# Optimization experiments

Hardware: AMD Instinct MI355X
Metric: run time of the kernel (lower is better)

Reference implementation:

```python
import math
import jax, jax.numpy as jnp
import numpy as np

S, D = 4096, 2048
H, DH = 16, 128
ROPE_BASE = 10000.0


def _rotate_half(x):
    # x: [..., dh]; pairs (x1, x2) -> (-x2, x1), interleaved
    shp = x.shape
    x = x.reshape(*shp[:-1], shp[-1] // 2, 2)
    x1, x2 = x[..., 0], x[..., 1]
    return jnp.stack((-x2, x1), axis=-1).reshape(shp)


def _rope_cos_sin(seq_len, dh):
    inv_freq = 1.0 / (ROPE_BASE ** (jnp.arange(0, dh, 2, dtype=jnp.float32) / dh))
    t = jnp.arange(seq_len, dtype=jnp.float32)
    freqs = jnp.einsum('i,j->ij', t, inv_freq)  # [S, dh/2]
    cos = jnp.repeat(jnp.cos(freqs), 2, axis=-1)  # [S, dh]
    sin = jnp.repeat(jnp.sin(freqs), 2, axis=-1)
    return cos, sin


def setup_inputs() -> dict:
    key = jax.random.key(0)
    kx, kq, kk, kv, ko = jax.random.split(key, 5)
    scale_in = 1.0 / math.sqrt(D)
    scale_hd = 1.0 / math.sqrt(H * DH)
    return {
        'x': jax.random.normal(kx, (S, D), dtype=jnp.float32),
        'mask': jnp.tril(jnp.ones((S, S), dtype=bool)),  # causal
        'wq': jax.random.normal(kq, (H * DH, D), dtype=jnp.float32) * scale_in,
        'wk': jax.random.normal(kk, (H * DH, D), dtype=jnp.float32) * scale_in,
        'wv': jax.random.normal(kv, (H * DH, D), dtype=jnp.float32) * scale_in,
        'wo': jax.random.normal(ko, (D, H * DH), dtype=jnp.float32) * scale_hd,
    }


def reference(x, mask, wq, wk, wv, wo):
    s = x.shape[0]
    # QKV projections (Linear: y = W @ x per token) -> [h, S, dh]
    q = (x @ wq.T).reshape(s, H, DH).transpose(1, 0, 2)
    k = (x @ wk.T).reshape(s, H, DH).transpose(1, 0, 2)
    v = (x @ wv.T).reshape(s, H, DH).transpose(1, 0, 2)
    # RoPE
    cos, sin = _rope_cos_sin(s, DH)  # [S, dh] each
    q = q * cos[None] + _rotate_half(q) * sin[None]
    k = k * cos[None] + _rotate_half(k) * sin[None]
    # Attention
    sim = jnp.einsum('hid,hjd->hij', q, k) / math.sqrt(DH)  # [h, S, S]
    sim = jnp.where(mask[None], sim, -jnp.inf)
    attn = jax.nn.softmax(sim, axis=-1)
    out = jnp.einsum('hij,hjd->ihd', attn, v).reshape(s, H * DH)
    return out @ wo.T
```

## Files before the change

### kernel.cpp

```cpp
#include <hip/hip_runtime.h>
#include <stdint.h>

#define S_LEN 4096
#define D_MODEL 2048
#define NH 16
#define DH 128

typedef short s16x8 __attribute__((ext_vector_type(8)));
typedef short s16x2 __attribute__((ext_vector_type(2)));
typedef unsigned short u16;
typedef unsigned short u16x4 __attribute__((ext_vector_type(4)));
typedef float f32x4 __attribute__((ext_vector_type(4)));

__device__ __forceinline__ u16 f2bf(float f) {
  union { float f; uint32_t u; } v; v.f = f;
  uint32_t u = v.u;
  u += 0x7FFFu + ((u >> 16) & 1u);
  return (u16)(u >> 16);
}

__device__ __forceinline__ float bf2f(u16 b) {
  union { uint32_t u; float f; } v; v.u = ((uint32_t)b) << 16;
  return v.f;
}

__device__ __forceinline__ void async_copy16(const u16* g, u16* l) {
  __builtin_amdgcn_global_load_lds(
      (const __attribute__((address_space(1))) unsigned int*)g,
      (__attribute__((address_space(3))) unsigned int*)l, 16, 0, 0);
}

__global__ void prep_kernel(
    const float4* __restrict__ x,
    const float4* __restrict__ wq, const float4* __restrict__ wk,
    const float4* __restrict__ wv, const float4* __restrict__ wo,
    u16* __restrict__ xb, u16* __restrict__ wqb, u16* __restrict__ wkb,
    u16* __restrict__ wvb, u16* __restrict__ wob,
    float* __restrict__ ctab, float* __restrict__ stab)
{
  int b = blockIdx.x;
  if (b < 24576) {
    const float4* src; u16* dst; int i;
    if (b < 8192) {
      src = x; dst = xb; i = b * 256 + threadIdx.x;
    } else {
      int wb = b - 8192;
      int which = wb >> 12;
      src = which == 0 ? wq : which == 1 ? wk : which == 2 ? wv : wo;
      dst = which == 0 ? wqb : which == 1 ? wkb : which == 2 ? wvb : wob;
      i = (wb & 4095) * 256 + threadIdx.x;
    }
    float4 v = src[i];
    u16x4 o;
    o[0] = f2bf(v.x); o[1] = f2bf(v.y); o[2] = f2bf(v.z); o[3] = f2bf(v.w);
    *(u16x4*)(dst + (size_t)i * 4) = o;
  } else {
    int idx = (b - 24576) * 256 + threadIdx.x;
    int t = idx >> 6, p = idx & 63;
    float invf = powf(10000.0f, -(float)p / 64.0f);
    float th = (float)t * invf;
    ctab[idx] = cosf(th);
    stab[idx] = sinf(th);
  }
}

#define PH_LGK0() do { asm volatile("s_waitcnt lgkmcnt(0)" ::: "memory"); \
                       __builtin_amdgcn_sched_barrier(0); } while (0)

__device__ __forceinline__ void stage16k(const u16* __restrict__ src, u16* dstbase,
                                         const int K) {
  const int tid = threadIdx.x;
  int rr = tid >> 3;
  int gc = ((tid & 7) ^ (rr & 7)) << 3;
  const u16* s = src + (size_t)rr * K + gc;
  u16* d = dstbase + (tid << 3);
  async_copy16(s, d);
  async_copy16(s + (size_t)64 * K, d + 4096);
}

__device__ __forceinline__ void mma256x128(
    const u16* __restrict__ Ab, const u16* __restrict__ Bb,
    const int K, u16* lds, f32x4 (&acc)[4][4])
{
  const int tid = threadIdx.x;
  const int lane = tid & 63, quad = lane >> 4, l16 = lane & 15;
  const int w = tid >> 6, wr = w >> 1, wc = w & 1;

  u16* const A0 = lds;
  u16* const B0 = lds + 16384;
  u16* const A1 = lds + 24576;
  u16* const B1 = lds + 40960;
  const int NT = K >> 6;

  auto sA = [&](int t, u16* buf) {
    int tc = t < NT ? t : NT - 1;
    stage16k(Ab + ((size_t)tc << 6), buf, K);
    stage16k(Ab + (size_t)128 * K + ((size_t)tc << 6), buf + 8192, K);
  };
  auto sB = [&](int t, u16* buf) {
    int tc = t < NT ? t : NT - 1;
    stage16k(Bb + ((size_t)tc << 6), buf, K);
  };

  s16x8 aC[4][2], aN[4][2], bA[2][2], bB0[2][2], bB1[2][2];

  auto rdA = [&](const u16* buf, s16x8 (&a)[4][2]) {
#pragma unroll
    for (int mt = 0; mt < 4; ++mt) {
      int ra = (wr << 6) + (mt << 4) + l16;
#pragma unroll
      for (int ks = 0; ks < 2; ++ks)
        a[mt][ks] = *(const s16x8*)(buf + (ra << 6) + ((((ks << 2) + quad) ^ (ra & 7)) << 3));
    }
  };
  auto rdBh = [&](const u16* buf, int nh, s16x8 (&b)[2][2]) {
#pragma unroll
    for (int nt = 0; nt < 2; ++nt) {
      int rb = (wc << 6) + (((nh << 1) + nt) << 4) + l16;
#pragma unroll
      for (int ks = 0; ks < 2; ++ks)
        b[nt][ks] = *(const s16x8*)(buf + (rb << 6) + ((((ks << 2) + quad) ^ (rb & 7)) << 3));
    }
  };
  auto mmah = [&](s16x8 (&a)[4][2], s16x8 (&b)[2][2], int nh) {
#pragma unroll
    for (int mt = 0; mt < 4; ++mt)
#pragma unroll
      for (int nt = 0; nt < 2; ++nt)
#pragma unroll
        for (int ks = 0; ks < 2; ++ks)
          acc[mt][(nh << 1) + nt] = __builtin_amdgcn_mfma_f32_16x16x32_bf16(
              a[mt][ks], b[nt][ks], acc[mt][(nh << 1) + nt], 0, 0, 0);
  };

  sA(0, A0); sB(0, B0); sA(1, A1); sB(1, B1);
  asm volatile("s_waitcnt vmcnt(6)" ::: "memory");
  __builtin_amdgcn_s_barrier();
  rdA(A0, aC); rdBh(B0, 0, bA); rdBh(B0, 1, bB0);

  const int NI = K >> 7;
#pragma unroll 1
  for (int i = 0; i < NI; ++i) {
    const int t0 = 2 * i, t1 = 2 * i + 1;
    PH_LGK0();
    __builtin_amdgcn_s_setprio(1);
    mmah(aC, bA, 0);
    __builtin_amdgcn_s_setprio(0);
    asm volatile("s_waitcnt vmcnt(0)" ::: "memory");
    __builtin_amdgcn_s_barrier();
    __builtin_amdgcn_s_setprio(1);
    sA(t0 + 2, A0); sB(t0 + 2, B0);
    rdA(A1, aN); rdBh(B1, 0, bA); rdBh(B1, 1, bB1);
    mmah(aC, bB0, 1);
    __builtin_amdgcn_s_setprio(0);
    __builtin_amdgcn_s_barrier();
    PH_LGK0();
    __builtin_amdgcn_s_setprio(1);
    mmah(aN, bA, 0);
    __builtin_amdgcn_s_setprio(0);
    asm volatile("s_waitcnt vmcnt(0)" ::: "memory");
    __builtin_amdgcn_s_barrier();
    __builtin_amdgcn_s_setprio(1);
    sA(t1 + 2, A1); sB(t1 + 2, B1);
    if (i + 1 < NI) { rdA(A0, aC); rdBh(B0, 0, bA); rdBh(B0, 1, bB0); }
    mmah(aN, bB1, 1);
    __builtin_amdgcn_s_setprio(0);
    __builtin_amdgcn_s_barrier();
  }
}

__global__ __launch_bounds__(512) void gemm256_qkv(
    const u16* __restrict__ A,
    const u16* __restrict__ wqb, const u16* __restrict__ wkb, const u16* __restrict__ wvb,
    u16* __restrict__ qh, u16* __restrict__ kh, u16* __restrict__ vh,
    const float* __restrict__ ctab, const float* __restrict__ stab)
{
  __shared__ __align__(16) u16 lds[49152];
  const int tid = threadIdx.x;
  const int lane = tid & 63, quad = lane >> 4, l16 = lane & 15;
  const int w = tid >> 6, wr = w >> 1, wc = w & 1;
  const int m0 = blockIdx.x << 8;
  const int by = blockIdx.y;
  const int which = by >> 4;
  const int n0 = (by & 15) << 7;
  const u16* B = which == 0 ? wqb : which == 1 ? wkb : wvb;
  u16* outp = which == 0 ? qh : which == 1 ? kh : vh;

  f32x4 acc[4][4];
  f32x4 zero = {0.f, 0.f, 0.f, 0.f};
#pragma unroll
  for (int i = 0; i < 4; ++i)
#pragma unroll
    for (int j = 0; j < 4; ++j) acc[i][j] = zero;

  mma256x128(A + (size_t)m0 * D_MODEL, B + (size_t)n0 * D_MODEL, D_MODEL, lds, acc);

#pragma unroll
  for (int mt = 0; mt < 4; ++mt) {
    int rowg = m0 + (wr << 6) + (mt << 4) + (quad << 2);
#pragma unroll
    for (int nt = 0; nt < 4; ++nt) {
      int cl = n0 + (wc << 6) + (nt << 4) + l16;
      int hh = cl >> 7, dd = cl & 127;
      int p = dd >> 1;
      f32x4 v = acc[mt][nt];
#pragma unroll
      for (int r = 0; r < 4; ++r) {
        float val = v[r];
        if (which < 2) {
          float partner = __shfl_xor(val, 1);
          float c = ctab[(size_t)(rowg + r) * 64 + p];
          float s = stab[(size_t)(rowg + r) * 64 + p];
          val = (dd & 1) ? fmaf(val, c, partner * s) : fmaf(val, c, -partner * s);
        }
        outp[((size_t)hh * S_LEN + (rowg + r)) * DH + dd] = f2bf(val);
      }
    }
  }
}

__global__ __launch_bounds__(512) void gemm256_out(
    const u16* __restrict__ A, const u16* __restrict__ B, float* __restrict__ outF)
{
  __shared__ __align__(16) u16 lds[49152];
  const int tid = threadIdx.x;
  const int lane = tid & 63, quad = lane >> 4, l16 = lane & 15;
  const int w = tid >> 6, wr = w >> 1, wc = w & 1;
  const int m0 = blockIdx.x << 8, n0 = blockIdx.y << 7;

  f32x4 acc[4][4];
  f32x4 zero = {0.f, 0.f, 0.f, 0.f};
#pragma unroll
  for (int i = 0; i < 4; ++i)
#pragma unroll
    for (int j = 0; j < 4; ++j) acc[i][j] = zero;

  mma256x128(A + (size_t)m0 * D_MODEL, B + (size_t)n0 * D_MODEL, D_MODEL, lds, acc);

#pragma unroll
  for (int mt = 0; mt < 4; ++mt) {
    int rowg = m0 + (wr << 6) + (mt << 4) + (quad << 2);
#pragma unroll
    for (int nt = 0; nt < 4; ++nt) {
      int col = n0 + (wc << 6) + (nt << 4) + l16;
      f32x4 v = acc[mt][nt];
#pragma unroll
      for (int r = 0; r < 4; ++r) outF[(size_t)(rowg + r) * D_MODEL + col] = v[r];
    }
  }
}

__global__ __launch_bounds__(512) void attn_kernel(
    const u16* __restrict__ Q, const u16* __restrict__ Kb,
    const u16* __restrict__ V,
    u16* __restrict__ U0, u16* __restrict__ U1, float* __restrict__ lbuf)
{
  __shared__ __align__(16) u16 lk[2][64 * 128];
  __shared__ __align__(16) u16 lvt[2][128 * 64];
  __shared__ __align__(16) u16 lp[8 * 2048];

  const int tid = threadIdx.x;
  const int w = tid >> 6, lane = tid & 63, quad = lane >> 4, l16 = lane & 15;
  const int linear = blockIdx.x;
  const int slot = linear >> 3;
  const int h = ((linear & 7) << 1) | (slot >> 4);
  const int bx = slot & 15;

  const u16* Qh = Q + (size_t)h * S_LEN * DH;
  const u16* Kh = Kb + (size_t)h * S_LEN * DH;
  const u16* Vh = V + (size_t)h * S_LEN * DH;

  const float scale = 0.08838834764831845f;
  const s16x8 vones = {0x3F80, 0x3F80, 0x3F80, 0x3F80, 0x3F80, 0x3F80, 0x3F80, 0x3F80};
  f32x4 zero = {0.f, 0.f, 0.f, 0.f};
  u16* lpw = lp + (w << 11);

  for (int seg = 0; seg < 2; ++seg) {
    const int qt = seg ? bx : (15 - bx);
    const int jlo = seg ? (2 * qt + 2) : 0;
    const int jhi = seg ? (4 * qt + 4) : (2 * qt + 2);
    const int i0 = qt << 8;
    const int iws = i0 + (w << 5);

    s16x8 qf[2][4];
#pragma unroll
    for (int s = 0; s < 2; ++s)
#pragma unroll
      for (int ks = 0; ks < 4; ++ks)
        qf[s][ks] = *(const s16x8*)(Qh + (size_t)(iws + (s << 4) + l16) * DH + ks * 32 + quad * 8);

    f32x4 accO[2][8];
#pragma unroll
    for (int s = 0; s < 2; ++s)
#pragma unroll
      for (int dt = 0; dt < 8; ++dt) accO[s][dt] = zero;
    f32x4 accL[2] = {zero, zero};

    {
      const int j0 = jlo << 6;
      int u = tid & 31, c8 = tid >> 5, r0 = u << 1;
      s16x8 v0 = *(const s16x8*)(Vh + (size_t)(j0 + r0) * DH + (c8 << 3));
      s16x8 v1 = *(const s16x8*)(Vh + (size_t)(j0 + r0 + 1) * DH + (c8 << 3));
#pragma unroll
      for (int rnd = 0; rnd < 2; ++rnd) {
        int c = rnd * 512 + tid;
        int r = c >> 4, cc = c & 15;
        int gcol = ((cc ^ (r & 15)) << 3);
        async_copy16(Kh + (size_t)(j0 + r) * DH + gcol, lk[0] + ((rnd * 512 + w * 64) << 3));
      }
      int cc = r0 >> 3;
#pragma unroll
      for (int e = 0; e < 8; ++e) {
        int d = (c8 << 3) + e;
        int off = (d << 6) + ((cc ^ (d & 7)) << 3) + (r0 & 7);
        s16x2 pr = {v0[e], v1[e]};
        *(s16x2*)(lvt[0] + off) = pr;
      }
    }
    __syncthreads();

    int cur = 0;
    for (int jt = jlo; jt < jhi; ++jt) {
      const int j0 = jt << 6;
      const bool has_next = (jt + 1) < jhi;

      s16x8 nv0, nv1;
      if (has_next) {
        const int nj0 = (jt + 1) << 6;
        int u = tid & 31, c8 = tid >> 5, r0 = u << 1;
        nv0 = *(const s16x8*)(Vh + (size_t)(nj0 + r0) * DH + (c8 << 3));
        nv1 = *(const s16x8*)(Vh + (size_t)(nj0 + r0 + 1) * DH + (c8 << 3));
#pragma unroll
        for (int rnd = 0; rnd < 2; ++rnd) {
          int c = rnd * 512 + tid;
          int r = c >> 4, cc = c & 15;
          int gcol = ((cc ^ (r & 15)) << 3);
          async_copy16(Kh + (size_t)(nj0 + r) * DH + gcol,
                       lk[cur ^ 1] + ((rnd * 512 + w * 64) << 3));
        }
      }

      const u16* lkc = lk[cur];
      f32x4 sa[2][4];
#pragma unroll
      for (int s = 0; s < 2; ++s)
#pragma unroll
        for (int nt = 0; nt < 4; ++nt) sa[s][nt] = zero;
      __builtin_amdgcn_s_setprio(1);
#pragma unroll
      for (int ks = 0; ks < 4; ++ks) {
#pragma unroll
        for (int nt = 0; nt < 4; ++nt) {
          int row = (nt << 4) + l16;
          s16x8 kf = *(const s16x8*)(lkc + (row << 7) + ((((ks << 2) + quad) ^ (row & 15)) << 3));
          sa[0][nt] = __builtin_amdgcn_mfma_f32_16x16x32_bf16(qf[0][ks], kf, sa[0][nt], 0, 0, 0);
          sa[1][nt] = __builtin_amdgcn_mfma_f32_16x16x32_bf16(qf[1][ks], kf, sa[1][nt], 0, 0, 0);
        }
      }
      __builtin_amdgcn_s_setprio(0);

#pragma unroll
      for (int s = 0; s < 2; ++s) {
        const int iw = iws + (s << 4);
        const bool maskt = (j0 + 63 > iw);
        u16* lps = lpw + (s << 10);
#pragma unroll
        for (int nt = 0; nt < 4; ++nt) {
          int col = (nt << 4) + l16;
          int j = j0 + col;
          int ccp = col >> 3;
#pragma unroll
          for (int r = 0; r < 4; ++r) {
            float raw = sa[s][nt][r];
            if (maskt) {
              int i = iw + (quad << 2) + r;
              if (j > i) raw = -1.0e30f;
            }
            float p = __expf(fmaf(raw, scale, -8.0f));
            union { float f; uint32_t u; } pv; pv.f = p;
            int m = (quad << 2) + r;
            lps[(m << 6) + ((ccp ^ (m & 7)) << 3) + (col & 7)] = (u16)(pv.u >> 16);
          }
        }
      }
      asm volatile("s_waitcnt lgkmcnt(0)" ::: "memory");
      s16x8 pf[2][2];
#pragma unroll
      for (int s = 0; s < 2; ++s)
#pragma unroll
        for (int kp = 0; kp < 2; ++kp)
          pf[s][kp] = *(const s16x8*)(lpw + (s << 10) + (l16 << 6) +
                                      ((((kp << 2) + quad) ^ (l16 & 7)) << 3));

      if (has_next) {
        int u = tid & 31, c8 = tid >> 5, r0 = u << 1;
        int cc = r0 >> 3;
        u16* dst = lvt[cur ^ 1];
#pragma unroll
        for (int e = 0; e < 8; ++e) {
          int d = (c8 << 3) + e;
          int off = (d << 6) + ((cc ^ (d & 7)) << 3) + (r0 & 7);
          s16x2 pr = {nv0[e], nv1[e]};
          *(s16x2*)(dst + off) = pr;
        }
      }

      const u16* lvc = lvt[cur];
      __builtin_amdgcn_s_setprio(1);
      accL[0] = __builtin_amdgcn_mfma_f32_16x16x32_bf16(pf[0][0], vones, accL[0], 0, 0, 0);
      accL[0] = __builtin_amdgcn_mfma_f32_16x16x32_bf16(pf[0][1], vones, accL[0], 0, 0, 0);
      accL[1] = __builtin_amdgcn_mfma_f32_16x16x32_bf16(pf[1][0], vones, accL[1], 0, 0, 0);
      accL[1] = __builtin_amdgcn_mfma_f32_16x16x32_bf16(pf[1][1], vones, accL[1], 0, 0, 0);
#pragma unroll
      for (int dt = 0; dt < 8; ++dt) {
#pragma unroll
        for (int kp = 0; kp < 2; ++kp) {
          int row = (dt << 4) + l16;
          s16x8 vf = *(const s16x8*)(lvc + (row << 6) + ((((kp << 2) + quad) ^ (row & 7)) << 3));
          accO[0][dt] = __builtin_amdgcn_mfma_f32_16x16x32_bf16(pf[0][kp], vf, accO[0][dt], 0, 0, 0);
          accO[1][dt] = __builtin_amdgcn_mfma_f32_16x16x32_bf16(pf[1][kp], vf, accO[1][dt], 0, 0, 0);
        }
      }
      __builtin_amdgcn_s_setprio(0);

      __syncthreads();
      cur ^= 1;
    }

    u16* Useg = seg ? U1 : U0;
    float* ls = lbuf + (size_t)seg * NH * S_LEN + (size_t)h * S_LEN;
#pragma unroll
    for (int s = 0; s < 2; ++s) {
      const int iw = iws + (s << 4);
#pragma unroll
      for (int r = 0; r < 4; ++r) {
        float lr = accL[s][r];
        float inv = lr > 0.f ? 1.0f / lr : 0.f;
        int srow = iw + (quad << 2) + r;
#pragma unroll
        for (int dt = 0; dt < 8; ++dt)
          Useg[((size_t)h * S_LEN + srow) * DH + (dt << 4) + l16] = f2bf(accO[s][dt][r] * inv);
        if (l16 == 0) ls[srow] = lr;
      }
    }
  }
}

__global__ void combine_kernel(const u16* __restrict__ U0, const u16* __restrict__ U1,
                               const float* __restrict__ lbuf, u16* __restrict__ ob)
{
  int t = blockIdx.x * 256 + threadIdx.x;
  int d8 = t & 15;
  int h = (t >> 4) & 15;
  int s = t >> 8;
  float l0 = lbuf[(size_t)h * S_LEN + s];
  float l1 = lbuf[(size_t)(NH * S_LEN) + (size_t)h * S_LEN + s];
  float inv = 1.0f / (l0 + l1);
  float w0 = l0 * inv, w1 = l1 * inv;
  size_t base = ((size_t)h * S_LEN + s) * DH + d8 * 8;
  s16x8 u0 = *(const s16x8*)(U0 + base);
  s16x8 u1 = *(const s16x8*)(U1 + base);
  u16 o[8];
#pragma unroll
  for (int e = 0; e < 8; ++e)
    o[e] = f2bf(w0 * bf2f((u16)u0[e]) + w1 * bf2f((u16)u1[e]));
  *(s16x8*)(ob + ((size_t)s * D_MODEL + h * DH + d8 * 8)) = *(s16x8*)o;
}

extern "C" void kernel_launch(void* const* d_in, const int* in_sizes, int n_in,
                              void* d_out, int out_size, void* d_ws, size_t ws_size,
                              hipStream_t stream) {
  const float* x  = (const float*)d_in[0];
  const float* wq = (const float*)d_in[2];
  const float* wk = (const float*)d_in[3];
  const float* wv = (const float*)d_in[4];
  const float* wo = (const float*)d_in[5];
  float* out = (float*)d_out;

  char* ws = (char*)d_ws;
  u16* xb  = (u16*)(ws);
  u16* wqb = (u16*)(ws + (16ull << 20));
  u16* wkb = (u16*)(ws + (24ull << 20));
  u16* wvb = (u16*)(ws + (32ull << 20));
  u16* wob = (u16*)(ws + (40ull << 20));
  u16* qh  = (u16*)(ws + (48ull << 20));
  u16* kh  = (u16*)(ws + (64ull << 20));
  u16* vh  = (u16*)(ws + (80ull << 20));
  float* ctab = (float*)(ws + (96ull << 20));
  float* stab = (float*)(ws + (97ull << 20));
  u16* U0 = (u16*)(ws);
  u16* U1 = (u16*)(ws + (16ull << 20));
  float* lbuf = (float*)(ws + (32ull << 20));
  u16* ob = qh;

  prep_kernel<<<25600, 256, 0, stream>>>(
      (const float4*)x, (const float4*)wq, (const float4*)wk,
      (const float4*)wv, (const float4*)wo,
      xb, wqb, wkb, wvb, wob, ctab, stab);

  gemm256_qkv<<<dim3(S_LEN / 256, 3 * D_MODEL / 128), 512, 0, stream>>>(
      xb, wqb, wkb, wvb, qh, kh, vh, ctab, stab);

  attn_kernel<<<dim3(256), 512, 0, stream>>>(qh, kh, vh, U0, U1, lbuf);
  combine_kernel<<<S_LEN * NH * 16 / 256, 256, 0, stream>>>(U0, U1, lbuf, ob);

  gemm256_out<<<dim3(S_LEN / 256, D_MODEL / 128), 512, 0, stream>>>(
      ob, wob, out);
}
```

Before: 430.1 us.

## Keep softmax probabilities in registers by transposing QK^T MFMA operands

Swaps the MFMA operand order so the score tile comes out transposed, and permutes the K rows each lane reads (with a matching new LDS swizzle) so each lane's accumulator values line up with the B-operand layout the PV MFMA needs. The probabilities are packed straight into registers, removing the per-wave LDS scratch buffer, its stores, the lgkmcnt wait and the reloads. This cuts LDS traffic and shared memory use, which may allow more occupancy. It also switches from truncation to round-to-nearest bf16 conversion, adding a few ALU ops per element.

```diff
diff --git a/kernel.cpp b/kernel.cpp
--- a/kernel.cpp
+++ b/kernel.cpp
@@ -257,7 +257,6 @@
 {
   __shared__ __align__(16) u16 lk[2][64 * 128];
   __shared__ __align__(16) u16 lvt[2][128 * 64];
-  __shared__ __align__(16) u16 lp[8 * 2048];
 
   const int tid = threadIdx.x;
   const int w = tid >> 6, lane = tid & 63, quad = lane >> 4, l16 = lane & 15;
@@ -273,7 +272,6 @@
   const float scale = 0.08838834764831845f;
   const s16x8 vones = {0x3F80, 0x3F80, 0x3F80, 0x3F80, 0x3F80, 0x3F80, 0x3F80, 0x3F80};
   f32x4 zero = {0.f, 0.f, 0.f, 0.f};
-  u16* lpw = lp + (w << 11);
 
   for (int seg = 0; seg < 2; ++seg) {
     const int qt = seg ? bx : (15 - bx);
@@ -305,7 +303,8 @@
       for (int rnd = 0; rnd < 2; ++rnd) {
         int c = rnd * 512 + tid;
         int r = c >> 4, cc = c & 15;
-        int gcol = ((cc ^ (r & 15)) << 3);
+        int hs = (r & 3) | (((r >> 3) & 3) << 2);
+        int gcol = ((cc ^ hs) << 3);
         async_copy16(Kh + (size_t)(j0 + r) * DH + gcol, lk[0] + ((rnd * 512 + w * 64) << 3));
       }
       int cc = r0 >> 3;
@@ -334,7 +333,8 @@
         for (int rnd = 0; rnd < 2; ++rnd) {
           int c = rnd * 512 + tid;
           int r = c >> 4, cc = c & 15;
-          int gcol = ((cc ^ (r & 15)) << 3);
+          int hs = (r & 3) | (((r >> 3) & 3) << 2);
+          int gcol = ((cc ^ hs) << 3);
           async_copy16(Kh + (size_t)(nj0 + r) * DH + gcol,
                        lk[cur ^ 1] + ((rnd * 512 + w * 64) << 3));
         }
@@ -351,46 +351,32 @@
       for (int ks = 0; ks < 4; ++ks) {
 #pragma unroll
         for (int nt = 0; nt < 4; ++nt) {
-          int row = (nt << 4) + l16;
-          s16x8 kf = *(const s16x8*)(lkc + (row << 7) + ((((ks << 2) + quad) ^ (row & 15)) << 3));
-          sa[0][nt] = __builtin_amdgcn_mfma_f32_16x16x32_bf16(qf[0][ks], kf, sa[0][nt], 0, 0, 0);
-          sa[1][nt] = __builtin_amdgcn_mfma_f32_16x16x32_bf16(qf[1][ks], kf, sa[1][nt], 0, 0, 0);
+          int row = ((nt >> 1) << 5) + ((l16 >> 2) << 3) + ((nt & 1) << 2) + (l16 & 3);
+          s16x8 kf = *(const s16x8*)(lkc + (row << 7) + ((((ks << 2) + quad) ^ l16) << 3));
+          sa[0][nt] = __builtin_amdgcn_mfma_f32_16x16x32_bf16(kf, qf[0][ks], sa[0][nt], 0, 0, 0);
+          sa[1][nt] = __builtin_amdgcn_mfma_f32_16x16x32_bf16(kf, qf[1][ks], sa[1][nt], 0, 0, 0);
         }
       }
       __builtin_amdgcn_s_setprio(0);
 
+      s16x8 pf[2][2];
 #pragma unroll
       for (int s = 0; s < 2; ++s) {
-        const int iw = iws + (s << 4);
-        const bool maskt = (j0 + 63 > iw);
-        u16* lps = lpw + (s << 10);
+        const int iq = iws + (s << 4) + l16;
+        const bool maskt = (j0 + 63 > iws + (s << 4));
 #pragma unroll
         for (int nt = 0; nt < 4; ++nt) {
-          int col = (nt << 4) + l16;
-          int j = j0 + col;
-          int ccp = col >> 3;
+          const int jb = j0 + ((nt >> 1) << 5) + (quad << 3) + ((nt & 1) << 2);
+          const int kp = nt >> 1, eb = (nt & 1) << 2;
 #pragma unroll
           for (int r = 0; r < 4; ++r) {
             float raw = sa[s][nt][r];
-            if (maskt) {
-              int i = iw + (quad << 2) + r;
-              if (j > i) raw = -1.0e30f;
-            }
+            if (maskt && (jb + r > iq)) raw = -1.0e30f;
             float p = __expf(fmaf(raw, scale, -8.0f));
-            union { float f; uint32_t u; } pv; pv.f = p;
-            int m = (quad << 2) + r;
-            lps[(m << 6) + ((ccp ^ (m & 7)) << 3) + (col & 7)] = (u16)(pv.u >> 16);
+            pf[s][kp][eb + r] = (short)f2bf(p);
           }
         }
       }
-      asm volatile("s_waitcnt lgkmcnt(0)" ::: "memory");
-      s16x8 pf[2][2];
-#pragma unroll
-      for (int s = 0; s < 2; ++s)
-#pragma unroll
-        for (int kp = 0; kp < 2; ++kp)
-          pf[s][kp] = *(const s16x8*)(lpw + (s << 10) + (l16 << 6) +
-                                      ((((kp << 2) + quad) ^ (l16 & 7)) << 3));
 
       if (has_next) {
         int u = tid & 31, c8 = tid >> 5, r0 = u << 1;
```

After: 441.2 us. +2.6%, slower.
